# Optimization experiments

Hardware: AMD Instinct MI355X
Metric: run time of the kernel (lower is better)

The kernel has to match this reference:

```python
import jax, jax.numpy as jnp
import numpy as np

D_MODEL, JOINT_DIM, VOCAB = 512, 640, 1024
B, T, U = 4, 256, 64


def setup_inputs() -> dict:
    key = jax.random.key(0)
    ks = jax.random.split(key, 8)
    s_in = 1.0 / np.sqrt(D_MODEL)
    s_j = 1.0 / np.sqrt(JOINT_DIM)
    return {
        "enc": jax.random.normal(ks[0], (B, T, D_MODEL), jnp.float32),
        "pred": jax.random.normal(ks[1], (B, U, D_MODEL), jnp.float32),
        "enc_w": jax.random.uniform(ks[2], (JOINT_DIM, D_MODEL), jnp.float32, -s_in, s_in),
        "enc_b": jax.random.uniform(ks[3], (JOINT_DIM,), jnp.float32, -s_in, s_in),
        "pred_w": jax.random.uniform(ks[4], (JOINT_DIM, D_MODEL), jnp.float32, -s_in, s_in),
        "pred_b": jax.random.uniform(ks[5], (JOINT_DIM,), jnp.float32, -s_in, s_in),
        "out_w": jax.random.uniform(ks[6], (VOCAB, JOINT_DIM), jnp.float32, -s_j, s_j),
        "out_b": jax.random.uniform(ks[7], (VOCAB,), jnp.float32, -s_j, s_j),
    }


def reference(enc, pred, enc_w, enc_b, pred_w, pred_b, out_w, out_b):
    # project encoder (B,T,J) and predictor (B,U,J)
    e = jnp.einsum("btd,jd->btj", enc, enc_w) + enc_b
    p = jnp.einsum("bud,jd->buj", pred, pred_w) + pred_b
    # broadcast add over the (T,U) grid, tanh, then vocab projection
    z = jnp.tanh(e[:, :, None, :] + p[:, None, :, :])  # (B,T,U,J)
    logits = jnp.einsum("btuj,vj->btuv", z, out_w) + out_b  # (B,T,U,V)
    return logits
```

## Files before the change

kernel.cpp:

```cpp
#include <hip/hip_runtime.h>
#include <cstdint>
#include <cstddef>


typedef __attribute__((ext_vector_type(8))) __bf16 bf16x8;
typedef __attribute__((ext_vector_type(4))) float f32x4;

__device__ __forceinline__ int swz(int row, int kElem) {
  return (row << 6) + (kElem ^ ((row & 7) << 3));
}

__device__ __forceinline__ float fast_tanh(float x) {
  float e = __builtin_amdgcn_exp2f(x * 2.88539008177793f);
  return 1.0f - 2.0f * __builtin_amdgcn_rcpf(e + 1.0f);
}

__device__ __forceinline__ void gload_lds16(const void* g, void* l) {
  __builtin_amdgcn_global_load_lds(
      (const __attribute__((address_space(1))) void*)g,
      (__attribute__((address_space(3))) void*)l, 16, 0, 0);
}

__device__ void proj_tile(const float* __restrict__ A, const float* __restrict__ W,
                          const float* __restrict__ bias, float* __restrict__ C,
                          int mt, int nt, __bf16* As, __bf16* Bs)
{
  const int tid  = threadIdx.x;
  const int r = tid & 127, half = tid >> 7;
  const int lane = tid & 63, wv = tid >> 6;
  const int wm = wv >> 1, wn = wv & 1;

  const float* arow = A + (size_t)(mt * 128 + r) * 512 + half * 32;
  const float* wrow = W + (size_t)(nt * 128 + r) * 512 + half * 32;

  f32x4 acc[4][4] = {};

  for (int k0 = 0; k0 < 512; k0 += 64) {
#pragma unroll
    for (int s = 0; s < 4; ++s) {
      f32x4 a0 = *(const f32x4*)(arow + k0 + s * 8);
      f32x4 a1 = *(const f32x4*)(arow + k0 + s * 8 + 4);
      f32x4 w0 = *(const f32x4*)(wrow + k0 + s * 8);
      f32x4 w1 = *(const f32x4*)(wrow + k0 + s * 8 + 4);
      bf16x8 za, zw;
#pragma unroll
      for (int j = 0; j < 4; ++j) {
        za[j] = (__bf16)a0[j]; za[4 + j] = (__bf16)a1[j];
        zw[j] = (__bf16)w0[j]; zw[4 + j] = (__bf16)w1[j];
      }
      const int kk = half * 32 + s * 8;
      *(bf16x8*)&As[swz(r, kk)] = za;
      *(bf16x8*)&Bs[swz(r, kk)] = zw;
    }
    __syncthreads();
#pragma unroll
    for (int kk = 0; kk < 2; ++kk) {
      bf16x8 af[4], bfr[4];
#pragma unroll
      for (int i = 0; i < 4; ++i) {
        af[i]  = *(const bf16x8*)&As[swz(wm * 64 + i * 16 + (lane & 15), kk * 32 + (lane >> 4) * 8)];
        bfr[i] = *(const bf16x8*)&Bs[swz(wn * 64 + i * 16 + (lane & 15), kk * 32 + (lane >> 4) * 8)];
      }
#pragma unroll
      for (int mi = 0; mi < 4; ++mi)
#pragma unroll
        for (int ni = 0; ni < 4; ++ni)
          acc[mi][ni] = __builtin_amdgcn_mfma_f32_16x16x32_bf16(af[mi], bfr[ni], acc[mi][ni], 0, 0, 0);
    }
    __syncthreads();
  }

  const int rowbase = mt * 128 + wm * 64;
  const int colbase = nt * 128 + wn * 64;
#pragma unroll
  for (int ni = 0; ni < 4; ++ni) {
    const int col = colbase + ni * 16 + (lane & 15);
    const float bb = bias[col];
#pragma unroll
    for (int mi = 0; mi < 4; ++mi) {
      const int row = rowbase + mi * 16 + (lane >> 4) * 4;
#pragma unroll
      for (int rg = 0; rg < 4; ++rg)
        C[(size_t)(row + rg) * 640 + col] = acc[mi][ni][rg] + bb;
    }
  }
}

__global__ __launch_bounds__(256) void prep_kernel(
    const float* __restrict__ enc,  const float* __restrict__ enc_w,  const float* __restrict__ enc_b,
    const float* __restrict__ pred, const float* __restrict__ pred_w, const float* __restrict__ pred_b,
    const float* __restrict__ out_w,
    float* __restrict__ E, float* __restrict__ P, __bf16* __restrict__ Wb)
{
  __shared__ __align__(16) __bf16 As[128 * 64];
  __shared__ __align__(16) __bf16 Bs[128 * 64];
  const int bid = blockIdx.x;
  if (bid < 40) {
    proj_tile(enc, enc_w, enc_b, E, bid / 5, bid % 5, As, Bs);
  } else if (bid < 50) {
    proj_tile(pred, pred_w, pred_b, P, (bid - 40) / 5, (bid - 40) % 5, As, Bs);
  } else {
    const int gid = (bid - 50) * 256 + threadIdx.x;
    const int v  = gid / 80;
    const int j8 = gid % 80;
    f32x4 w0 = *(const f32x4*)(out_w + (size_t)v * 640 + j8 * 8);
    f32x4 w1 = *(const f32x4*)(out_w + (size_t)v * 640 + j8 * 8 + 4);
    bf16x8 z;
#pragma unroll
    for (int j = 0; j < 4; ++j) { z[j] = (__bf16)w0[j]; z[4 + j] = (__bf16)w1[j]; }
    const int nb = v >> 8, rr = v & 255;
    const int kb = j8 >> 3, kk = (j8 & 7) * 8;
    *(bf16x8*)(Wb + ((size_t)(nb * 10 + kb) << 14) + swz(rr, kk)) = z;
  }
}

__global__ __launch_bounds__(512, 4) void joiner_main(
    const float* __restrict__ E, const float* __restrict__ P,
    const __bf16* __restrict__ Wb, const float* __restrict__ outb,
    float* __restrict__ out)
{
  __shared__ __align__(16) __bf16 As[128 * 64];
  __shared__ __align__(16) __bf16 Bs[256 * 64];
  const int tid = threadIdx.x;
  const int nt = blockIdx.x & 3;
  const int mt = blockIdx.x >> 2;
  const int row0 = mt << 7;
  const int b  = row0 >> 14;
  const int t0 = (row0 >> 6) & 255;
  const int r = tid & 127, q = tid >> 7;
  const int lane = tid & 63, wv = tid >> 6;
  const int wm = wv >> 2, wn = wv & 3;

  const float* ep = E + (size_t)((b << 8) + t0 + (r >> 6)) * 640;
  const float* pp = P + (size_t)((b << 6) + (r & 63)) * 640;
  const __bf16* wsrc = Wb + ((size_t)(nt * 10) << 14);

  f32x4 acc[4][4] = {};

  for (int kt = 0; kt < 10; ++kt) {
    const int k0 = kt << 6;
#pragma unroll
    for (int c = 0; c < 4; ++c) {
      const int off = c * 4096 + wv * 512;
      gload_lds16(wsrc + (kt << 14) + off + lane * 8, &Bs[off]);
    }
#pragma unroll
    for (int g = 0; g < 2; ++g) {
      const int kk = g * 32 + q * 8;
      f32x4 e0 = *(const f32x4*)(ep + k0 + kk);
      f32x4 e1 = *(const f32x4*)(ep + k0 + kk + 4);
      f32x4 p0 = *(const f32x4*)(pp + k0 + kk);
      f32x4 p1 = *(const f32x4*)(pp + k0 + kk + 4);
      bf16x8 z;
#pragma unroll
      for (int j = 0; j < 4; ++j) {
        z[j]     = (__bf16)fast_tanh(e0[j] + p0[j]);
        z[4 + j] = (__bf16)fast_tanh(e1[j] + p1[j]);
      }
      *(bf16x8*)&As[swz(r, kk)] = z;
    }
    __syncthreads();
#pragma unroll
    for (int kk = 0; kk < 2; ++kk) {
      bf16x8 af[4], bfr[4];
#pragma unroll
      for (int i = 0; i < 4; ++i) {
        af[i]  = *(const bf16x8*)&As[swz(wm * 64 + i * 16 + (lane & 15), kk * 32 + (lane >> 4) * 8)];
        bfr[i] = *(const bf16x8*)&Bs[swz(wn * 64 + i * 16 + (lane & 15), kk * 32 + (lane >> 4) * 8)];
      }
#pragma unroll
      for (int mi = 0; mi < 4; ++mi)
#pragma unroll
        for (int ni = 0; ni < 4; ++ni)
          acc[mi][ni] = __builtin_amdgcn_mfma_f32_16x16x32_bf16(af[mi], bfr[ni], acc[mi][ni], 0, 0, 0);
    }
    __syncthreads();
  }

  const int rowbase = row0 + wm * 64;
  const int colbase = (nt << 8) + wn * 64;
#pragma unroll
  for (int ni = 0; ni < 4; ++ni) {
    const int col = colbase + ni * 16 + (lane & 15);
    const float bb = outb[col];
#pragma unroll
    for (int mi = 0; mi < 4; ++mi) {
      const int row = rowbase + mi * 16 + (lane >> 4) * 4;
#pragma unroll
      for (int rg = 0; rg < 4; ++rg)
        out[(size_t)(row + rg) * 1024 + col] = acc[mi][ni][rg] + bb;
    }
  }
}

extern "C" void kernel_launch(void* const* d_in, const int* in_sizes, int n_in,
                              void* d_out, int out_size, void* d_ws, size_t ws_size,
                              hipStream_t stream) {
  const float* enc    = (const float*)d_in[0];
  const float* pred   = (const float*)d_in[1];
  const float* enc_w  = (const float*)d_in[2];
  const float* enc_b  = (const float*)d_in[3];
  const float* pred_w = (const float*)d_in[4];
  const float* pred_b = (const float*)d_in[5];
  const float* out_w  = (const float*)d_in[6];
  const float* out_b  = (const float*)d_in[7];
  float* out = (float*)d_out;

  char* ws = (char*)d_ws;
  float*  E  = (float*)(ws);
  float*  P  = (float*)(ws + 2621440);
  __bf16* Wb = (__bf16*)(ws + 3276800);

  prep_kernel<<<dim3(370), dim3(256), 0, stream>>>(
      enc, enc_w, enc_b, pred, pred_w, pred_b, out_w, E, P, Wb);
  joiner_main<<<dim3(512 * 4), dim3(512), 0, stream>>>(E, P, Wb, out_b, out);
}
```

Before: 187.0 us.

## Double-buffer LDS tiles in joiner main loop to overlap loads with MFMA

```diff
diff --git a/kernel.cpp b/kernel.cpp
--- a/kernel.cpp
+++ b/kernel.cpp
@@ -114,13 +114,13 @@
   }
 }
 
-__global__ __launch_bounds__(512, 4) void joiner_main(
+__global__ __launch_bounds__(512, 2) void joiner_main(
     const float* __restrict__ E, const float* __restrict__ P,
     const __bf16* __restrict__ Wb, const float* __restrict__ outb,
     float* __restrict__ out)
 {
-  __shared__ __align__(16) __bf16 As[128 * 64];
-  __shared__ __align__(16) __bf16 Bs[256 * 64];
+  __shared__ __align__(16) __bf16 As[2 * 128 * 64];
+  __shared__ __align__(16) __bf16 Bs[2 * 256 * 64];
   const int tid = threadIdx.x;
   const int nt = blockIdx.x & 3;
   const int mt = blockIdx.x >> 2;
@@ -136,46 +136,73 @@
   const __bf16* wsrc = Wb + ((size_t)(nt * 10) << 14);
 
   f32x4 acc[4][4] = {};
-
-  for (int kt = 0; kt < 10; ++kt) {
-    const int k0 = kt << 6;
+  f32x4 eA[2], eB[2], pA[2], pB[2];
+
+  auto loadEP = [&](int k0) {
+#pragma unroll
+    for (int g = 0; g < 2; ++g) {
+      const int kk = k0 + g * 32 + q * 8;
+      eA[g] = *(const f32x4*)(ep + kk);
+      eB[g] = *(const f32x4*)(ep + kk + 4);
+      pA[g] = *(const f32x4*)(pp + kk);
+      pB[g] = *(const f32x4*)(pp + kk + 4);
+    }
+  };
+  auto writeA = [&](__bf16* Asb) {
+#pragma unroll
+    for (int g = 0; g < 2; ++g) {
+      bf16x8 z;
+#pragma unroll
+      for (int j = 0; j < 4; ++j) {
+        z[j]     = (__bf16)fast_tanh(eA[g][j] + pA[g][j]);
+        z[4 + j] = (__bf16)fast_tanh(eB[g][j] + pB[g][j]);
+      }
+      *(bf16x8*)&Asb[swz(r, g * 32 + q * 8)] = z;
+    }
+  };
+  auto stageB = [&](int kt, __bf16* Bsb) {
 #pragma unroll
     for (int c = 0; c < 4; ++c) {
       const int off = c * 4096 + wv * 512;
-      gload_lds16(wsrc + (kt << 14) + off + lane * 8, &Bs[off]);
-    }
-#pragma unroll
-    for (int g = 0; g < 2; ++g) {
-      const int kk = g * 32 + q * 8;
-      f32x4 e0 = *(const f32x4*)(ep + k0 + kk);
-      f32x4 e1 = *(const f32x4*)(ep + k0 + kk + 4);
-      f32x4 p0 = *(const f32x4*)(pp + k0 + kk);
-      f32x4 p1 = *(const f32x4*)(pp + k0 + kk + 4);
-      bf16x8 z;
-#pragma unroll
-      for (int j = 0; j < 4; ++j) {
-        z[j]     = (__bf16)fast_tanh(e0[j] + p0[j]);
-        z[4 + j] = (__bf16)fast_tanh(e1[j] + p1[j]);
-      }
-      *(bf16x8*)&As[swz(r, kk)] = z;
-    }
-    __syncthreads();
+      gload_lds16(wsrc + (kt << 14) + off + lane * 8, &Bsb[off]);
+    }
+  };
+  auto compute = [&](const __bf16* Asb, const __bf16* Bsb) {
 #pragma unroll
     for (int kk = 0; kk < 2; ++kk) {
       bf16x8 af[4], bfr[4];
 #pragma unroll
       for (int i = 0; i < 4; ++i) {
-        af[i]  = *(const bf16x8*)&As[swz(wm * 64 + i * 16 + (lane & 15), kk * 32 + (lane >> 4) * 8)];
-        bfr[i] = *(const bf16x8*)&Bs[swz(wn * 64 + i * 16 + (lane & 15), kk * 32 + (lane >> 4) * 8)];
-      }
+        af[i]  = *(const bf16x8*)&Asb[swz(wm * 64 + i * 16 + (lane & 15), kk * 32 + (lane >> 4) * 8)];
+        bfr[i] = *(const bf16x8*)&Bsb[swz(wn * 64 + i * 16 + (lane & 15), kk * 32 + (lane >> 4) * 8)];
+      }
+      __builtin_amdgcn_s_setprio(1);
 #pragma unroll
       for (int mi = 0; mi < 4; ++mi)
 #pragma unroll
         for (int ni = 0; ni < 4; ++ni)
           acc[mi][ni] = __builtin_amdgcn_mfma_f32_16x16x32_bf16(af[mi], bfr[ni], acc[mi][ni], 0, 0, 0);
-    }
+      __builtin_amdgcn_s_setprio(0);
+    }
+  };
+
+  loadEP(0);
+  stageB(0, Bs);
+  writeA(As);
+  __syncthreads();
+
+  int cur = 0;
+  for (int kt = 0; kt < 9; ++kt) {
+    __bf16* Asn = As + (cur ^ 1) * 8192;
+    __bf16* Bsn = Bs + (cur ^ 1) * 16384;
+    stageB(kt + 1, Bsn);
+    loadEP((kt + 1) << 6);
+    compute(As + cur * 8192, Bs + cur * 16384);
+    writeA(Asn);
     __syncthreads();
-  }
+    cur ^= 1;
+  }
+  compute(As + cur * 8192, Bs + cur * 16384);
 
   const int rowbase = row0 + wm * 64;
   const int colbase = (nt << 8) + wn * 64;
```

Measured after the change: 270.7 us. 44.8% more time.

## Double-buffer joiner tiles, enlarge M tile to 256, interleave tanh with MFMA

Applied to the files above, without the earlier changes.

```diff
diff --git a/kernel.cpp b/kernel.cpp
--- a/kernel.cpp
+++ b/kernel.cpp
@@ -114,77 +114,223 @@
   }
 }
 
-__global__ __launch_bounds__(512, 4) void joiner_main(
+__global__ __launch_bounds__(512, 2) void joiner_main(
     const float* __restrict__ E, const float* __restrict__ P,
     const __bf16* __restrict__ Wb, const float* __restrict__ outb,
     float* __restrict__ out)
 {
-  __shared__ __align__(16) __bf16 As[128 * 64];
-  __shared__ __align__(16) __bf16 Bs[256 * 64];
+  __shared__ __align__(16) __bf16 As[2][16384];
+  __shared__ __align__(16) __bf16 Bs[2][16384];
   const int tid = threadIdx.x;
   const int nt = blockIdx.x & 3;
   const int mt = blockIdx.x >> 2;
-  const int row0 = mt << 7;
+  const int row0 = mt << 8;
   const int b  = row0 >> 14;
   const int t0 = (row0 >> 6) & 255;
-  const int r = tid & 127, q = tid >> 7;
   const int lane = tid & 63, wv = tid >> 6;
   const int wm = wv >> 2, wn = wv & 3;
 
-  const float* ep = E + (size_t)((b << 8) + t0 + (r >> 6)) * 640;
-  const float* pp = P + (size_t)((b << 6) + (r & 63)) * 640;
+  const int ar = tid & 255;
+  const int h  = tid >> 8;
+  const float* ep = E + (size_t)((b << 8) + t0 + (ar >> 6)) * 640 + h * 32;
+  const float* pp = P + (size_t)((b << 6) + (ar & 63)) * 640 + h * 32;
   const __bf16* wsrc = Wb + ((size_t)(nt * 10) << 14);
 
-  f32x4 acc[4][4] = {};
-
-  for (int kt = 0; kt < 10; ++kt) {
-    const int k0 = kt << 6;
-#pragma unroll
-    for (int c = 0; c < 4; ++c) {
-      const int off = c * 4096 + wv * 512;
-      gload_lds16(wsrc + (kt << 14) + off + lane * 8, &Bs[off]);
-    }
-#pragma unroll
-    for (int g = 0; g < 2; ++g) {
-      const int kk = g * 32 + q * 8;
-      f32x4 e0 = *(const f32x4*)(ep + k0 + kk);
-      f32x4 e1 = *(const f32x4*)(ep + k0 + kk + 4);
-      f32x4 p0 = *(const f32x4*)(pp + k0 + kk);
-      f32x4 p1 = *(const f32x4*)(pp + k0 + kk + 4);
-      bf16x8 z;
+  const int arow = wm * 128 + (lane & 15);
+  const int brow = wn * 64  + (lane & 15);
+  const int kcol = (lane >> 4) * 8;
+
+  f32x4 acc[8][4] = {};
+  bf16x8 bfr[4][2];
+  f32x4 ec[4], pc[4];
+
+#pragma unroll
+  for (int c = 0; c < 4; ++c)
+    gload_lds16(wsrc + c * 4096 + wv * 512 + lane * 8, &Bs[0][c * 4096 + wv * 512]);
+#pragma unroll
+  for (int c = 0; c < 2; ++c) {
+#pragma unroll
+    for (int i = 0; i < 4; ++i) {
+      ec[i] = *(const f32x4*)(ep + c * 16 + i * 4);
+      pc[i] = *(const f32x4*)(pp + c * 16 + i * 4);
+    }
+    bf16x8 z0, z1;
+#pragma unroll
+    for (int j = 0; j < 4; ++j) {
+      z0[j]     = (__bf16)fast_tanh(ec[0][j] + pc[0][j]);
+      z0[4 + j] = (__bf16)fast_tanh(ec[1][j] + pc[1][j]);
+      z1[j]     = (__bf16)fast_tanh(ec[2][j] + pc[2][j]);
+      z1[4 + j] = (__bf16)fast_tanh(ec[3][j] + pc[3][j]);
+    }
+    *(bf16x8*)&As[0][swz(ar, h * 32 + c * 16)]     = z0;
+    *(bf16x8*)&As[0][swz(ar, h * 32 + c * 16 + 8)] = z1;
+  }
+  asm volatile("s_waitcnt vmcnt(0) lgkmcnt(0)" ::: "memory");
+  __builtin_amdgcn_s_barrier();
+
+  for (int kt = 0; kt < 9; ++kt) {
+    const int cur = kt & 1;
+    const __bf16* Asc = As[cur];
+    const __bf16* Bsc = Bs[cur];
+    __bf16* Asn = As[cur ^ 1];
+    __bf16* Bsn = Bs[cur ^ 1];
+    const int knext = (kt + 1) << 6;
+    bf16x8 af[2][2];
+
+#pragma unroll
+    for (int c = 0; c < 4; ++c)
+      gload_lds16(wsrc + ((size_t)(kt + 1) << 14) + c * 4096 + wv * 512 + lane * 8,
+                  &Bsn[c * 4096 + wv * 512]);
+#pragma unroll
+    for (int ni = 0; ni < 4; ++ni)
+#pragma unroll
+      for (int kk = 0; kk < 2; ++kk)
+        bfr[ni][kk] = *(const bf16x8*)&Bsc[swz(brow + ni * 16, kcol + kk * 32)];
+#pragma unroll
+    for (int lm = 0; lm < 2; ++lm)
+#pragma unroll
+      for (int kk = 0; kk < 2; ++kk)
+        af[lm][kk] = *(const bf16x8*)&Asc[swz(arow + lm * 16, kcol + kk * 32)];
+    __builtin_amdgcn_s_barrier();
+    asm volatile("s_waitcnt lgkmcnt(0)" ::: "memory");
+    __builtin_amdgcn_sched_barrier(0);
+    __builtin_amdgcn_s_setprio(1);
+#pragma unroll
+    for (int kk = 0; kk < 2; ++kk)
+#pragma unroll
+      for (int lm = 0; lm < 2; ++lm)
+#pragma unroll
+        for (int ni = 0; ni < 4; ++ni)
+          acc[lm][ni] = __builtin_amdgcn_mfma_f32_16x16x32_bf16(af[lm][kk], bfr[ni][kk], acc[lm][ni], 0, 0, 0);
+    __builtin_amdgcn_s_setprio(0);
+    __builtin_amdgcn_s_barrier();
+
+#pragma unroll
+    for (int i = 0; i < 4; ++i) {
+      ec[i] = *(const f32x4*)(ep + knext + i * 4);
+      pc[i] = *(const f32x4*)(pp + knext + i * 4);
+    }
+#pragma unroll
+    for (int lm = 0; lm < 2; ++lm)
+#pragma unroll
+      for (int kk = 0; kk < 2; ++kk)
+        af[lm][kk] = *(const bf16x8*)&Asc[swz(arow + (2 + lm) * 16, kcol + kk * 32)];
+    __builtin_amdgcn_s_barrier();
+    asm volatile("s_waitcnt lgkmcnt(0)" ::: "memory");
+    __builtin_amdgcn_sched_barrier(0);
+    __builtin_amdgcn_s_setprio(1);
+#pragma unroll
+    for (int kk = 0; kk < 2; ++kk)
+#pragma unroll
+      for (int lm = 0; lm < 2; ++lm)
+#pragma unroll
+        for (int ni = 0; ni < 4; ++ni)
+          acc[2 + lm][ni] = __builtin_amdgcn_mfma_f32_16x16x32_bf16(af[lm][kk], bfr[ni][kk], acc[2 + lm][ni], 0, 0, 0);
+    __builtin_amdgcn_s_setprio(0);
+    __builtin_amdgcn_s_barrier();
+
+#pragma unroll
+    for (int lm = 0; lm < 2; ++lm)
+#pragma unroll
+      for (int kk = 0; kk < 2; ++kk)
+        af[lm][kk] = *(const bf16x8*)&Asc[swz(arow + (4 + lm) * 16, kcol + kk * 32)];
+    {
+      bf16x8 z0, z1;
 #pragma unroll
       for (int j = 0; j < 4; ++j) {
-        z[j]     = (__bf16)fast_tanh(e0[j] + p0[j]);
-        z[4 + j] = (__bf16)fast_tanh(e1[j] + p1[j]);
+        z0[j]     = (__bf16)fast_tanh(ec[0][j] + pc[0][j]);
+        z0[4 + j] = (__bf16)fast_tanh(ec[1][j] + pc[1][j]);
+        z1[j]     = (__bf16)fast_tanh(ec[2][j] + pc[2][j]);
+        z1[4 + j] = (__bf16)fast_tanh(ec[3][j] + pc[3][j]);
       }
-      *(bf16x8*)&As[swz(r, kk)] = z;
-    }
-    __syncthreads();
-#pragma unroll
-    for (int kk = 0; kk < 2; ++kk) {
-      bf16x8 af[4], bfr[4];
-#pragma unroll
-      for (int i = 0; i < 4; ++i) {
-        af[i]  = *(const bf16x8*)&As[swz(wm * 64 + i * 16 + (lane & 15), kk * 32 + (lane >> 4) * 8)];
-        bfr[i] = *(const bf16x8*)&Bs[swz(wn * 64 + i * 16 + (lane & 15), kk * 32 + (lane >> 4) * 8)];
+      *(bf16x8*)&Asn[swz(ar, h * 32)]     = z0;
+      *(bf16x8*)&Asn[swz(ar, h * 32 + 8)] = z1;
+    }
+#pragma unroll
+    for (int i = 0; i < 4; ++i) {
+      ec[i] = *(const f32x4*)(ep + knext + 16 + i * 4);
+      pc[i] = *(const f32x4*)(pp + knext + 16 + i * 4);
+    }
+    asm volatile("s_waitcnt lgkmcnt(0)" ::: "memory");
+    __builtin_amdgcn_s_barrier();
+    __builtin_amdgcn_sched_barrier(0);
+    __builtin_amdgcn_s_setprio(1);
+#pragma unroll
+    for (int kk = 0; kk < 2; ++kk)
+#pragma unroll
+      for (int lm = 0; lm < 2; ++lm)
+#pragma unroll
+        for (int ni = 0; ni < 4; ++ni)
+          acc[4 + lm][ni] = __builtin_amdgcn_mfma_f32_16x16x32_bf16(af[lm][kk], bfr[ni][kk], acc[4 + lm][ni], 0, 0, 0);
+    __builtin_amdgcn_s_setprio(0);
+    __builtin_amdgcn_s_barrier();
+
+#pragma unroll
+    for (int lm = 0; lm < 2; ++lm)
+#pragma unroll
+      for (int kk = 0; kk < 2; ++kk)
+        af[lm][kk] = *(const bf16x8*)&Asc[swz(arow + (6 + lm) * 16, kcol + kk * 32)];
+    {
+      bf16x8 z0, z1;
+#pragma unroll
+      for (int j = 0; j < 4; ++j) {
+        z0[j]     = (__bf16)fast_tanh(ec[0][j] + pc[0][j]);
+        z0[4 + j] = (__bf16)fast_tanh(ec[1][j] + pc[1][j]);
+        z1[j]     = (__bf16)fast_tanh(ec[2][j] + pc[2][j]);
+        z1[4 + j] = (__bf16)fast_tanh(ec[3][j] + pc[3][j]);
       }
-#pragma unroll
-      for (int mi = 0; mi < 4; ++mi)
-#pragma unroll
-        for (int ni = 0; ni < 4; ++ni)
-          acc[mi][ni] = __builtin_amdgcn_mfma_f32_16x16x32_bf16(af[mi], bfr[ni], acc[mi][ni], 0, 0, 0);
-    }
-    __syncthreads();
-  }
-
-  const int rowbase = row0 + wm * 64;
+      *(bf16x8*)&Asn[swz(ar, h * 32 + 16)] = z0;
+      *(bf16x8*)&Asn[swz(ar, h * 32 + 24)] = z1;
+    }
+    asm volatile("s_waitcnt vmcnt(0) lgkmcnt(0)" ::: "memory");
+    __builtin_amdgcn_s_barrier();
+    __builtin_amdgcn_sched_barrier(0);
+    __builtin_amdgcn_s_setprio(1);
+#pragma unroll
+    for (int kk = 0; kk < 2; ++kk)
+#pragma unroll
+      for (int lm = 0; lm < 2; ++lm)
+#pragma unroll
+        for (int ni = 0; ni < 4; ++ni)
+          acc[6 + lm][ni] = __builtin_amdgcn_mfma_f32_16x16x32_bf16(af[lm][kk], bfr[ni][kk], acc[6 + lm][ni], 0, 0, 0);
+    __builtin_amdgcn_s_setprio(0);
+    __builtin_amdgcn_s_barrier();
+  }
+
+  {
+    const __bf16* Asc = As[1];
+    const __bf16* Bsc = Bs[1];
+    bf16x8 af[2][2];
+#pragma unroll
+    for (int ni = 0; ni < 4; ++ni)
+#pragma unroll
+      for (int kk = 0; kk < 2; ++kk)
+        bfr[ni][kk] = *(const bf16x8*)&Bsc[swz(brow + ni * 16, kcol + kk * 32)];
+#pragma unroll
+    for (int p = 0; p < 4; ++p) {
+#pragma unroll
+      for (int lm = 0; lm < 2; ++lm)
+#pragma unroll
+        for (int kk = 0; kk < 2; ++kk)
+          af[lm][kk] = *(const bf16x8*)&Asc[swz(arow + (2 * p + lm) * 16, kcol + kk * 32)];
+#pragma unroll
+      for (int kk = 0; kk < 2; ++kk)
+#pragma unroll
+        for (int lm = 0; lm < 2; ++lm)
+#pragma unroll
+          for (int ni = 0; ni < 4; ++ni)
+            acc[2 * p + lm][ni] = __builtin_amdgcn_mfma_f32_16x16x32_bf16(af[lm][kk], bfr[ni][kk], acc[2 * p + lm][ni], 0, 0, 0);
+    }
+  }
+
+  const int rowbase = row0 + wm * 128;
   const int colbase = (nt << 8) + wn * 64;
 #pragma unroll
   for (int ni = 0; ni < 4; ++ni) {
     const int col = colbase + ni * 16 + (lane & 15);
     const float bb = outb[col];
 #pragma unroll
-    for (int mi = 0; mi < 4; ++mi) {
+    for (int mi = 0; mi < 8; ++mi) {
       const int row = rowbase + mi * 16 + (lane >> 4) * 4;
 #pragma unroll
       for (int rg = 0; rg < 4; ++rg)
@@ -213,5 +359,5 @@
 
   prep_kernel<<<dim3(370), dim3(256), 0, stream>>>(
       enc, enc_w, enc_b, pred, pred_w, pred_b, out_w, E, P, Wb);
-  joiner_main<<<dim3(512 * 4), dim3(512), 0, stream>>>(E, P, Wb, out_b, out);
-}
+  joiner_main<<<dim3(1024), dim3(512), 0, stream>>>(E, P, Wb, out_b, out);
+}
```

Measured after the change: 234.5 us. 25.4% more time.

## Store projections in bf16 and double-buffer the weight tile with prefetch

Applied to the files above, without the earlier changes.

```diff
diff --git a/kernel.cpp b/kernel.cpp
--- a/kernel.cpp
+++ b/kernel.cpp
@@ -22,7 +22,7 @@
 }
 
 __device__ void proj_tile(const float* __restrict__ A, const float* __restrict__ W,
-                          const float* __restrict__ bias, float* __restrict__ C,
+                          const float* __restrict__ bias, __bf16* __restrict__ C,
                           int mt, int nt, __bf16* As, __bf16* Bs)
 {
   const int tid  = threadIdx.x;
@@ -81,7 +81,7 @@
       const int row = rowbase + mi * 16 + (lane >> 4) * 4;
 #pragma unroll
       for (int rg = 0; rg < 4; ++rg)
-        C[(size_t)(row + rg) * 640 + col] = acc[mi][ni][rg] + bb;
+        C[(size_t)(row + rg) * 640 + col] = (__bf16)(acc[mi][ni][rg] + bb);
     }
   }
 }
@@ -90,7 +90,7 @@
     const float* __restrict__ enc,  const float* __restrict__ enc_w,  const float* __restrict__ enc_b,
     const float* __restrict__ pred, const float* __restrict__ pred_w, const float* __restrict__ pred_b,
     const float* __restrict__ out_w,
-    float* __restrict__ E, float* __restrict__ P, __bf16* __restrict__ Wb)
+    __bf16* __restrict__ E, __bf16* __restrict__ P, __bf16* __restrict__ Wb)
 {
   __shared__ __align__(16) __bf16 As[128 * 64];
   __shared__ __align__(16) __bf16 Bs[128 * 64];
@@ -115,67 +115,91 @@
 }
 
 __global__ __launch_bounds__(512, 4) void joiner_main(
-    const float* __restrict__ E, const float* __restrict__ P,
+    const __bf16* __restrict__ E, const __bf16* __restrict__ P,
     const __bf16* __restrict__ Wb, const float* __restrict__ outb,
     float* __restrict__ out)
 {
-  __shared__ __align__(16) __bf16 As[128 * 64];
-  __shared__ __align__(16) __bf16 Bs[256 * 64];
+  __shared__ __align__(16) __bf16 As[8192];
+  __shared__ __align__(16) __bf16 Bs[2][16384];
   const int tid = threadIdx.x;
   const int nt = blockIdx.x & 3;
   const int mt = blockIdx.x >> 2;
   const int row0 = mt << 7;
   const int b  = row0 >> 14;
   const int t0 = (row0 >> 6) & 255;
-  const int r = tid & 127, q = tid >> 7;
+  const int ar = tid & 127, h = tid >> 7;
   const int lane = tid & 63, wv = tid >> 6;
   const int wm = wv >> 2, wn = wv & 3;
 
-  const float* ep = E + (size_t)((b << 8) + t0 + (r >> 6)) * 640;
-  const float* pp = P + (size_t)((b << 6) + (r & 63)) * 640;
+  const __bf16* ep = E + (size_t)((b << 8) + t0 + (ar >> 6)) * 640 + h * 16;
+  const __bf16* pp = P + (size_t)((b << 6) + (ar & 63)) * 640 + h * 16;
   const __bf16* wsrc = Wb + ((size_t)(nt * 10) << 14);
 
   f32x4 acc[4][4] = {};
-
-  for (int kt = 0; kt < 10; ++kt) {
-    const int k0 = kt << 6;
-#pragma unroll
-    for (int c = 0; c < 4; ++c) {
-      const int off = c * 4096 + wv * 512;
-      gload_lds16(wsrc + (kt << 14) + off + lane * 8, &Bs[off]);
-    }
-#pragma unroll
-    for (int g = 0; g < 2; ++g) {
-      const int kk = g * 32 + q * 8;
-      f32x4 e0 = *(const f32x4*)(ep + k0 + kk);
-      f32x4 e1 = *(const f32x4*)(ep + k0 + kk + 4);
-      f32x4 p0 = *(const f32x4*)(pp + k0 + kk);
-      f32x4 p1 = *(const f32x4*)(pp + k0 + kk + 4);
+  bf16x8 eA[2], pA[2];
+
+  auto stageB = [&](int kt, __bf16* dst) {
+#pragma unroll
+    for (int c = 0; c < 4; ++c)
+      gload_lds16(wsrc + ((size_t)kt << 14) + c * 4096 + wv * 512 + lane * 8,
+                  dst + c * 4096 + wv * 512);
+  };
+  auto loadEP = [&](int k0) {
+#pragma unroll
+    for (int c = 0; c < 2; ++c) {
+      eA[c] = *(const bf16x8*)(ep + k0 + c * 8);
+      pA[c] = *(const bf16x8*)(pp + k0 + c * 8);
+    }
+  };
+  auto writeA = [&]() {
+#pragma unroll
+    for (int c = 0; c < 2; ++c) {
       bf16x8 z;
 #pragma unroll
-      for (int j = 0; j < 4; ++j) {
-        z[j]     = (__bf16)fast_tanh(e0[j] + p0[j]);
-        z[4 + j] = (__bf16)fast_tanh(e1[j] + p1[j]);
-      }
-      *(bf16x8*)&As[swz(r, kk)] = z;
-    }
-    __syncthreads();
+      for (int j = 0; j < 8; ++j)
+        z[j] = (__bf16)fast_tanh((float)eA[c][j] + (float)pA[c][j]);
+      *(bf16x8*)&As[swz(ar, h * 16 + c * 8)] = z;
+    }
+  };
+  auto compute = [&](const __bf16* Bsc) {
 #pragma unroll
     for (int kk = 0; kk < 2; ++kk) {
       bf16x8 af[4], bfr[4];
 #pragma unroll
       for (int i = 0; i < 4; ++i) {
         af[i]  = *(const bf16x8*)&As[swz(wm * 64 + i * 16 + (lane & 15), kk * 32 + (lane >> 4) * 8)];
-        bfr[i] = *(const bf16x8*)&Bs[swz(wn * 64 + i * 16 + (lane & 15), kk * 32 + (lane >> 4) * 8)];
+        bfr[i] = *(const bf16x8*)&Bsc[swz(wn * 64 + i * 16 + (lane & 15), kk * 32 + (lane >> 4) * 8)];
       }
+      asm volatile("s_waitcnt lgkmcnt(0)" ::: "memory");
+      __builtin_amdgcn_sched_barrier(0);
+      __builtin_amdgcn_s_setprio(1);
 #pragma unroll
       for (int mi = 0; mi < 4; ++mi)
 #pragma unroll
         for (int ni = 0; ni < 4; ++ni)
           acc[mi][ni] = __builtin_amdgcn_mfma_f32_16x16x32_bf16(af[mi], bfr[ni], acc[mi][ni], 0, 0, 0);
-    }
-    __syncthreads();
-  }
+      __builtin_amdgcn_s_setprio(0);
+    }
+  };
+
+  stageB(0, Bs[0]);
+  loadEP(0);
+  writeA();
+  asm volatile("s_waitcnt vmcnt(0) lgkmcnt(0)" ::: "memory");
+  __builtin_amdgcn_s_barrier();
+
+  for (int kt = 0; kt < 9; ++kt) {
+    const int cur = kt & 1;
+    stageB(kt + 1, Bs[cur ^ 1]);
+    loadEP((kt + 1) << 6);
+    compute(Bs[cur]);
+    __builtin_amdgcn_s_barrier();
+    __builtin_amdgcn_sched_barrier(0);
+    writeA();
+    asm volatile("s_waitcnt lgkmcnt(0)" ::: "memory");
+    __builtin_amdgcn_s_barrier();
+  }
+  compute(Bs[1]);
 
   const int rowbase = row0 + wm * 64;
   const int colbase = (nt << 8) + wn * 64;
@@ -207,11 +231,11 @@
   float* out = (float*)d_out;
 
   char* ws = (char*)d_ws;
-  float*  E  = (float*)(ws);
-  float*  P  = (float*)(ws + 2621440);
-  __bf16* Wb = (__bf16*)(ws + 3276800);
+  __bf16* E  = (__bf16*)(ws);
+  __bf16* P  = (__bf16*)(ws + 1310720);
+  __bf16* Wb = (__bf16*)(ws + 1638400);
 
   prep_kernel<<<dim3(370), dim3(256), 0, stream>>>(
       enc, enc_w, enc_b, pred, pred_w, pred_b, out_w, E, P, Wb);
-  joiner_main<<<dim3(512 * 4), dim3(512), 0, stream>>>(E, P, Wb, out_b, out);
-}
+  joiner_main<<<dim3(2048), dim3(512), 0, stream>>>(E, P, Wb, out_b, out);
+}
```

New measurement: 172.8 us. 1.08x faster.
